# Optimization experiments

Measured on AMD Instinct MI355X. Metric: run time of the kernel, lower is better.

## Reference

```python
import jax, jax.numpy as jnp
import numpy as np

B, S, D, K = 16, 4096, 256, 1024


def setup_inputs() -> dict:
    key = jax.random.key(0)
    k1, k2 = jax.random.split(key)
    z_e = jax.random.normal(k1, (B, S, D), dtype=jnp.float32)
    # nn.Embedding weight initialized uniform(-1/K, 1/K)
    codebook = jax.random.uniform(k2, (K, D), dtype=jnp.float32,
                                  minval=-1.0 / K, maxval=1.0 / K)
    return {"z_e": z_e, "codebook": codebook}


def reference(z_e, codebook):
    # straight_through path of VQEmbedding
    d = codebook.shape[1]
    x = z_e.reshape(-1, d)                                   # [N, D]
    dist = (jnp.sum(x * x, axis=1, keepdims=True)
            + jnp.sum(codebook * codebook, axis=1)
            - 2.0 * (x @ codebook.T))                        # [N, K]
    idx = jnp.argmin(dist, axis=1)                           # [N]
    codes = jnp.take(codebook, idx, axis=0).reshape(z_e.shape)  # gather
    z_q = z_e + jax.lax.stop_gradient(codes - z_e)           # straight-through codes (detached codebook)
    z_q_bar = codes                                          # codes with grad to codebook
    return (z_q, z_q_bar)
```

## Files before the change

kernel.cpp:

```cpp
#include <hip/hip_runtime.h>
#include <stdint.h>

#define D 256
#define KCODES 1024
#define NROWS 65536

using int4v  = __attribute__((ext_vector_type(4))) int;
using f32x4v = __attribute__((ext_vector_type(4))) float;

__device__ __forceinline__ float rne_f(float x) { return __builtin_rintf(x); }

__device__ __forceinline__ void gl_lds16(const void* g, void* l) {
  __builtin_amdgcn_global_load_lds(
      (const __attribute__((address_space(1))) void*)g,
      (__attribute__((address_space(3))) void*)l, 16, 0, 0);
}

__device__ __forceinline__ void dig4(float t, int* d) {
  float f0 = rne_f(t);  float t1 = __fmul_rn(__fsub_rn(t, f0), 256.0f);
  float f1 = rne_f(t1); float t2 = __fmul_rn(__fsub_rn(t1, f1), 256.0f);
  float f2 = rne_f(t2); float t3 = __fmul_rn(__fsub_rn(t2, f2), 256.0f);
  float f3 = rne_f(t3);
  int d0 = (int)f0, d1 = (int)f1, d2 = (int)f2, d3 = (int)f3;
  if (d3 == 128) { d3 = -128; ++d2; }
  if (d2 == 128) { d2 = -128; ++d1; }
  if (d1 == 128) { d1 = -128; ++d0; }
  d[0] = d0; d[1] = d1; d[2] = d2; d[3] = d3;
}

__device__ __forceinline__ float np_block128_sumsq(const float* __restrict__ q) {
  float r[8], v[8];
  *(float4*)(v) = *(const float4*)(q);
  *(float4*)(v + 4) = *(const float4*)(q + 4);
#pragma unroll
  for (int j = 0; j < 8; ++j) r[j] = __fmul_rn(v[j], v[j]);
  for (int i = 8; i < 128; i += 8) {
    *(float4*)(v) = *(const float4*)(q + i);
    *(float4*)(v + 4) = *(const float4*)(q + i + 4);
#pragma unroll
    for (int j = 0; j < 8; ++j) r[j] = __fadd_rn(r[j], __fmul_rn(v[j], v[j]));
  }
  float t01 = __fadd_rn(r[0], r[1]);
  float t23 = __fadd_rn(r[2], r[3]);
  float t45 = __fadd_rn(r[4], r[5]);
  float t67 = __fadd_rn(r[6], r[7]);
  return __fadd_rn(__fadd_rn(t01, t23), __fadd_rn(t45, t67));
}
__device__ __forceinline__ float np_sumsq256(const float* __restrict__ q) {
  return __fadd_rn(np_block128_sumsq(q), np_block128_sumsq(q + 128));
}

__global__ __launch_bounds__(256) void prep_all(const float* __restrict__ z,
                                                const float* __restrict__ cb,
                                                float* __restrict__ c2,
                                                float* __restrict__ srow,
                                                char* __restrict__ cbd) {
  __shared__ float zs[64][260];
  const int bid = blockIdx.x;
  const int tid = threadIdx.x;
  if (bid < 1040) {
    const float* src; float* dst; int r0;
    if (bid < 1024) { r0 = bid * 64; src = z; dst = srow; }
    else            { r0 = (bid - 1024) * 64; src = cb; dst = c2; }
#pragma unroll
    for (int it = 0; it < 16; ++it) {
      int g = tid + it * 256, row = g >> 6, f4 = g & 63;
      *(float4*)(&zs[row][f4 * 4]) = *(const float4*)(src + (size_t)(r0 + row) * D + f4 * 4);
    }
    __syncthreads();
    if (tid < 64) dst[r0 + tid] = np_sumsq256(&zs[tid][0]);
    return;
  }
  int id = (bid - 1040) * 256 + tid;
  int n = id >> 4, kc = id & 15;
  int f = kc >> 2, kg = kc & 3, nt = n >> 5, c = n & 31;
  const float* src = cb + (size_t)n * D + kc * 16;
  float v[16];
  *(float4*)(v) = *(const float4*)(src);
  *(float4*)(v + 4) = *(const float4*)(src + 4);
  *(float4*)(v + 8) = *(const float4*)(src + 8);
  *(float4*)(v + 12) = *(const float4*)(src + 12);
  int dg[16][4];
#pragma unroll
  for (int e = 0; e < 16; ++e) dig4(v[e] * 65536.0f, dg[e]);
  size_t base = (size_t)nt * 8192 + f * 2048 + (c >> 4) * 1024 + kg * 256 + (c & 15) * 16;
#pragma unroll
  for (int p = 0; p < 4; ++p) {
    int4v wv;
#pragma unroll
    for (int wi = 0; wi < 4; ++wi)
      wv[wi] = (dg[wi * 4][p] & 255) | ((dg[wi * 4 + 1][p] & 255) << 8) |
               ((dg[wi * 4 + 2][p] & 255) << 16) | (dg[wi * 4 + 3][p] << 24);
    *(int4v*)(cbd + (size_t)p * (KCODES * 256) + base) = wv;
  }
}

#define BM 64
#define BN 16
#define NT (KCODES / BN)

#define MFI16(a, b, c) __builtin_amdgcn_mfma_i32_16x16x64_i8((a), (b), (c), 0, 0, 0)

__global__ __launch_bounds__(256, 4) void vq_mfma(
    const float* __restrict__ z, const float* __restrict__ cb,
    const float* __restrict__ c2g, const float* __restrict__ srowg,
    const char* __restrict__ cbd, float* __restrict__ out) {
  __shared__ alignas(16) char bbuf[2][16384];
  __shared__ float c2s[KCODES];
  __shared__ int bidx_s[BM];

  const int tid = threadIdx.x;
  const int lane = tid & 63;
  const int w = tid >> 6;
  const int r0 = blockIdx.x * BM;
  const int l15 = lane & 15, l4 = lane >> 4;

  c2s[tid] = c2g[tid];
  c2s[tid + 256] = c2g[tid + 256];
  c2s[tid + 512] = c2g[tid + 512];
  c2s[tid + 768] = c2g[tid + 768];

  float sr[4];
#pragma unroll
  for (int r = 0; r < 4; ++r) sr[r] = srowg[r0 + w * 16 + l4 * 4 + r];

  int4v Adig[4][4];
  {
    const float* zr = z + (size_t)(r0 + w * 16 + l15) * D + l4 * 16;
#pragma unroll
    for (int f = 0; f < 4; ++f) {
      float v[16];
      *(float4*)(v) = *(const float4*)(zr + f * 64);
      *(float4*)(v + 4) = *(const float4*)(zr + f * 64 + 4);
      *(float4*)(v + 8) = *(const float4*)(zr + f * 64 + 8);
      *(float4*)(v + 12) = *(const float4*)(zr + f * 64 + 12);
      int dg[16][4];
#pragma unroll
      for (int e = 0; e < 16; ++e) dig4(v[e] * 16.0f, dg[e]);
#pragma unroll
      for (int p = 0; p < 4; ++p) {
        int4v wv;
#pragma unroll
        for (int wi = 0; wi < 4; ++wi)
          wv[wi] = (dg[wi * 4][p] & 255) | ((dg[wi * 4 + 1][p] & 255) << 8) |
                   ((dg[wi * 4 + 2][p] & 255) << 16) | (dg[wi * 4 + 3][p] << 24);
        Adig[p][f] = wv;
      }
    }
  }

  const char* cbd_b = cbd;
#define STAGE(ntv, dstbase) do { \
    const char* s_ = cbd_b + (size_t)((ntv) >> 1) * 8192 + (tid >> 6) * 2048 + \
                     ((ntv) & 1) * 1024 + (tid & 63) * 16; \
    char* d_ = (dstbase) + (tid >> 6) * 1024 + (tid & 63) * 16; \
    gl_lds16(s_,          d_); \
    gl_lds16(s_ + 262144, d_ + 4096); \
    gl_lds16(s_ + 524288, d_ + 8192); \
    gl_lds16(s_ + 786432, d_ + 12288); \
  } while (0)

  float bd[4]; int bi[4];
#pragma unroll
  for (int r = 0; r < 4; ++r) { bd[r] = 3.4e38f; bi[r] = 0x7fffffff; }

  int4v acc[4];

  STAGE(0, &bbuf[0][0]);
  __syncthreads();

  for (int nt = 0; nt < NT; ++nt) {
    const char* cur = &bbuf[nt & 1][0];
    if (nt + 1 < NT) STAGE(nt + 1, &bbuf[(nt + 1) & 1][0]);
#pragma unroll
    for (int s = 0; s < 4; ++s) { int4v zz = {0, 0, 0, 0}; acc[s] = zz; }
#pragma unroll
    for (int kf = 0; kf < 4; ++kf) {
      const char* pb = cur + kf * 1024 + lane * 16;
      int4v B0 = *(const int4v*)(pb);
      int4v B1 = *(const int4v*)(pb + 4096);
      int4v B2 = *(const int4v*)(pb + 8192);
      int4v B3 = *(const int4v*)(pb + 12288);
      acc[1] = MFI16(Adig[0][kf], B1, acc[1]);
      acc[3] = MFI16(Adig[0][kf], B3, acc[3]);
      acc[2] = MFI16(Adig[0][kf], B2, acc[2]);
      acc[1] = MFI16(Adig[1][kf], B0, acc[1]);
      acc[3] = MFI16(Adig[1][kf], B2, acc[3]);
      acc[2] = MFI16(Adig[1][kf], B1, acc[2]);
      acc[0] = MFI16(Adig[0][kf], B0, acc[0]);
      acc[3] = MFI16(Adig[2][kf], B1, acc[3]);
      acc[2] = MFI16(Adig[2][kf], B0, acc[2]);
      acc[3] = MFI16(Adig[3][kf], B0, acc[3]);
    }
    {
      const int kc = nt * BN + l15;
      const float c2v = c2s[kc];
#pragma unroll
      for (int r = 0; r < 4; ++r) {
        int hi32 = acc[0][r] * 256 + acc[1][r];
        double lo_d = fma((double)acc[2][r], 256.0, (double)acc[3][r]);
        double md = fma((double)hi32, 65536.0, lo_d) * 0x1p-44;
        float mf = (float)md;
        float dist = __fsub_rn(__fadd_rn(sr[r], c2v), __fmul_rn(2.0f, mf));
        if (dist < bd[r]) { bd[r] = dist; bi[r] = kc; }
      }
    }
    __syncthreads();
  }

#pragma unroll
  for (int r = 0; r < 4; ++r) {
#pragma unroll
    for (int m = 1; m < 16; m <<= 1) {
      float od = __shfl_xor(bd[r], m);
      int oi = __shfl_xor(bi[r], m);
      if (od < bd[r] || (od == bd[r] && oi < bi[r])) { bd[r] = od; bi[r] = oi; }
    }
    if (l15 == 0) bidx_s[w * 16 + l4 * 4 + r] = bi[r];
  }
  __syncthreads();

  {
    float* out0 = out;
    float* out1 = out + (size_t)NROWS * D;
#pragma unroll
    for (int rr = 0; rr < 16; ++rr) {
      const int row_l = w * 16 + rr;
      const int grow = r0 + row_l;
      const int kb = bidx_s[row_l];
      f32x4v c4 = *(const f32x4v*)(cb + (size_t)kb * D + lane * 4);
      f32x4v z4 = *(const f32x4v*)(z + (size_t)grow * D + lane * 4);
      f32x4v q;
      q.x = __fadd_rn(z4.x, __fsub_rn(c4.x, z4.x));
      q.y = __fadd_rn(z4.y, __fsub_rn(c4.y, z4.y));
      q.z = __fadd_rn(z4.z, __fsub_rn(c4.z, z4.z));
      q.w = __fadd_rn(z4.w, __fsub_rn(c4.w, z4.w));
      __builtin_nontemporal_store(q, (f32x4v*)(out0 + (size_t)grow * D + lane * 4));
      __builtin_nontemporal_store(c4, (f32x4v*)(out1 + (size_t)grow * D + lane * 4));
    }
  }
}

__global__ void c2_kernel_fb(const float* __restrict__ cb, float* __restrict__ c2) {
  int k = blockIdx.x * blockDim.x + threadIdx.x;
  if (k < KCODES) c2[k] = np_sumsq256(cb + (size_t)k * D);
}

__global__ __launch_bounds__(256) void vq_fallback(const float* __restrict__ z,
                                                   const float* __restrict__ cb,
                                                   const float* __restrict__ c2,
                                                   float* __restrict__ out) {
  __shared__ float zs[64][260];
  __shared__ float cs[64][260];
  __shared__ float srow[64];
  __shared__ int bidx[64];
  const int tid = threadIdx.x;
  const int tx = tid & 15, ty = tid >> 4;
  const int r0 = blockIdx.x * 64;
#pragma unroll
  for (int it = 0; it < 16; ++it) {
    int g = tid + it * 256, row = g >> 6, f4 = g & 63;
    *(float4*)(&zs[row][f4 * 4]) = *(const float4*)(z + (size_t)(r0 + row) * D + f4 * 4);
  }
  __syncthreads();
  if (tid < 64) srow[tid] = np_sumsq256(&zs[tid][0]);
  float bd[4]; int bi[4];
#pragma unroll
  for (int j = 0; j < 4; ++j) { bd[j] = 3.4e38f; bi[j] = 0x7fffffff; }
  for (int t = 0; t < KCODES / 64; ++t) {
    __syncthreads();
#pragma unroll
    for (int it = 0; it < 16; ++it) {
      int g = tid + it * 256, row = g >> 6, f4 = g & 63;
      *(float4*)(&cs[row][f4 * 4]) = *(const float4*)(cb + (size_t)(t * 64 + row) * D + f4 * 4);
    }
    __syncthreads();
    double acc[4][4];
#pragma unroll
    for (int j = 0; j < 4; ++j)
#pragma unroll
      for (int i = 0; i < 4; ++i) acc[j][i] = 0.0;
#pragma unroll 2
    for (int d = 0; d < D; d += 4) {
      float4 a[4], b[4];
#pragma unroll
      for (int j = 0; j < 4; ++j) a[j] = *(const float4*)(&zs[ty + 16 * j][d]);
#pragma unroll
      for (int i = 0; i < 4; ++i) b[i] = *(const float4*)(&cs[tx + 16 * i][d]);
#pragma unroll
      for (int j = 0; j < 4; ++j)
#pragma unroll
        for (int i = 0; i < 4; ++i) {
          acc[j][i] += (double)a[j].x * (double)b[i].x;
          acc[j][i] += (double)a[j].y * (double)b[i].y;
          acc[j][i] += (double)a[j].z * (double)b[i].z;
          acc[j][i] += (double)a[j].w * (double)b[i].w;
        }
    }
#pragma unroll
    for (int j = 0; j < 4; ++j) {
      const float s = srow[ty + 16 * j];
#pragma unroll
      for (int i = 0; i < 4; ++i) {
        const int k = t * 64 + tx + 16 * i;
        const float m = (float)acc[j][i];
        const float dist = __fsub_rn(__fadd_rn(s, c2[k]), __fmul_rn(2.0f, m));
        if (dist < bd[j]) { bd[j] = dist; bi[j] = k; }
      }
    }
  }
  __syncthreads();
  float* red_d = &cs[0][0];
  int* red_i = (int*)&cs[20][0];
#pragma unroll
  for (int j = 0; j < 4; ++j) {
    red_d[(ty + 16 * j) * 16 + tx] = bd[j];
    red_i[(ty + 16 * j) * 16 + tx] = bi[j];
  }
  __syncthreads();
  if (tid < 64) {
    float best = red_d[tid * 16 + 0];
    int bsti = red_i[tid * 16 + 0];
    for (int x = 1; x < 16; ++x) {
      float d2 = red_d[tid * 16 + x]; int i2 = red_i[tid * 16 + x];
      if (d2 < best || (d2 == best && i2 < bsti)) { best = d2; bsti = i2; }
    }
    bidx[tid] = bsti;
  }
  __syncthreads();
  const int wid = tid >> 6, lane = tid & 63;
  float* out0 = out;
  float* out1 = out + (size_t)NROWS * D;
  for (int r = wid; r < 64; r += 4) {
    const int gr = r0 + r;
    const int kb = bidx[r];
    float4 c4 = *(const float4*)(cb + (size_t)kb * D + lane * 4);
    float4 z4 = *(const float4*)(&zs[r][lane * 4]);
    float4 q;
    q.x = __fadd_rn(z4.x, __fsub_rn(c4.x, z4.x));
    q.y = __fadd_rn(z4.y, __fsub_rn(c4.y, z4.y));
    q.z = __fadd_rn(z4.z, __fsub_rn(c4.z, z4.z));
    q.w = __fadd_rn(z4.w, __fsub_rn(c4.w, z4.w));
    *(float4*)(out0 + (size_t)gr * D + lane * 4) = q;
    *(float4*)(out1 + (size_t)gr * D + lane * 4) = c4;
  }
}

extern "C" void kernel_launch(void* const* d_in, const int* in_sizes, int n_in,
                              void* d_out, int out_size, void* d_ws, size_t ws_size,
                              hipStream_t stream) {
  const float* z = (const float*)d_in[0];
  const float* cb = (const float*)d_in[1];
  float* out = (float*)d_out;

  const size_t c2_off = 0;
  const size_t srow_off = 4096;
  const size_t cbd_off = 4096 + 262144;
  const size_t need = cbd_off + (size_t)4 * KCODES * 256;

  if (ws_size < need) {
    float* c2 = (float*)d_ws;
    c2_kernel_fb<<<KCODES / 256, 256, 0, stream>>>(cb, c2);
    vq_fallback<<<NROWS / 64, 256, 0, stream>>>(z, cb, c2, out);
    return;
  }

  float* c2 = (float*)((char*)d_ws + c2_off);
  float* srow = (float*)((char*)d_ws + srow_off);
  char* cbd = (char*)d_ws + cbd_off;

  prep_all<<<1104, 256, 0, stream>>>(z, cb, c2, srow, cbd);
  vq_mfma<<<NROWS / BM, 256, 0, stream>>>(z, cb, c2, srow, cbd, out);
}
```

Baseline: 175.9 us.

## Load codebook digits directly from global memory instead of LDS double buffer

Removes the LDS double-buffered staging of the int8 codebook digit tiles (global_load_lds plus per-iteration barriers). Each wave now reads its B fragments straight from global memory, relying on L2/L1 caching because every block reads the same codebook. This drops the per-tile __syncthreads and frees 32KB of LDS. The trade-off is exposed global-load latency with no explicit prefetch, so the MFMA chain may stall on loads. Launch bounds are relaxed from 4 to 3 waves per SIMD.

```diff
diff --git a/kernel.cpp b/kernel.cpp
--- a/kernel.cpp
+++ b/kernel.cpp
@@ -9,12 +9,6 @@
 using f32x4v = __attribute__((ext_vector_type(4))) float;
 
 __device__ __forceinline__ float rne_f(float x) { return __builtin_rintf(x); }
-
-__device__ __forceinline__ void gl_lds16(const void* g, void* l) {
-  __builtin_amdgcn_global_load_lds(
-      (const __attribute__((address_space(1))) void*)g,
-      (__attribute__((address_space(3))) void*)l, 16, 0, 0);
-}
 
 __device__ __forceinline__ void dig4(float t, int* d) {
   float f0 = rne_f(t);  float t1 = __fmul_rn(__fsub_rn(t, f0), 256.0f);
@@ -101,11 +95,10 @@
 
 #define MFI16(a, b, c) __builtin_amdgcn_mfma_i32_16x16x64_i8((a), (b), (c), 0, 0, 0)
 
-__global__ __launch_bounds__(256, 4) void vq_mfma(
+__global__ __launch_bounds__(256, 3) void vq_mfma(
     const float* __restrict__ z, const float* __restrict__ cb,
     const float* __restrict__ c2g, const float* __restrict__ srowg,
     const char* __restrict__ cbd, float* __restrict__ out) {
-  __shared__ alignas(16) char bbuf[2][16384];
   __shared__ float c2s[KCODES];
   __shared__ int bidx_s[BM];
 
@@ -149,38 +142,26 @@
     }
   }
 
-  const char* cbd_b = cbd;
-#define STAGE(ntv, dstbase) do { \
-    const char* s_ = cbd_b + (size_t)((ntv) >> 1) * 8192 + (tid >> 6) * 2048 + \
-                     ((ntv) & 1) * 1024 + (tid & 63) * 16; \
-    char* d_ = (dstbase) + (tid >> 6) * 1024 + (tid & 63) * 16; \
-    gl_lds16(s_,          d_); \
-    gl_lds16(s_ + 262144, d_ + 4096); \
-    gl_lds16(s_ + 524288, d_ + 8192); \
-    gl_lds16(s_ + 786432, d_ + 12288); \
-  } while (0)
+  __syncthreads();
 
   float bd[4]; int bi[4];
 #pragma unroll
   for (int r = 0; r < 4; ++r) { bd[r] = 3.4e38f; bi[r] = 0x7fffffff; }
 
   int4v acc[4];
-
-  STAGE(0, &bbuf[0][0]);
-  __syncthreads();
+  const char* cbd_b = cbd + lane * 16;
 
   for (int nt = 0; nt < NT; ++nt) {
-    const char* cur = &bbuf[nt & 1][0];
-    if (nt + 1 < NT) STAGE(nt + 1, &bbuf[(nt + 1) & 1][0]);
+    const char* tb = cbd_b + (size_t)(nt >> 1) * 8192 + (nt & 1) * 1024;
 #pragma unroll
     for (int s = 0; s < 4; ++s) { int4v zz = {0, 0, 0, 0}; acc[s] = zz; }
 #pragma unroll
     for (int kf = 0; kf < 4; ++kf) {
-      const char* pb = cur + kf * 1024 + lane * 16;
-      int4v B0 = *(const int4v*)(pb);
-      int4v B1 = *(const int4v*)(pb + 4096);
-      int4v B2 = *(const int4v*)(pb + 8192);
-      int4v B3 = *(const int4v*)(pb + 12288);
+      const char* pk = tb + kf * 2048;
+      int4v B0 = *(const int4v*)(pk);
+      int4v B1 = *(const int4v*)(pk + 262144);
+      int4v B2 = *(const int4v*)(pk + 524288);
+      int4v B3 = *(const int4v*)(pk + 786432);
       acc[1] = MFI16(Adig[0][kf], B1, acc[1]);
       acc[3] = MFI16(Adig[0][kf], B3, acc[3]);
       acc[2] = MFI16(Adig[0][kf], B2, acc[2]);
@@ -205,7 +186,6 @@
         if (dist < bd[r]) { bd[r] = dist; bi[r] = kc; }
       }
     }
-    __syncthreads();
   }
 
 #pragma unroll
```

After: 348.6 us. +98.2%, slower.

## Triple-buffer codebook tiles in LDS with counted vmcnt waits and MFMA priority

Applied to the files above, without the earlier changes.

Replaces the double-buffered LDS staging of codebook digit tiles with a three-buffer ring that prefetches two tiles ahead. It waits with explicit s_waitcnt vmcnt(4) plus a raw s_barrier instead of a full __syncthreads, so the load for the next-but-one tile stays in flight across the barrier. The MFMA block is wrapped in s_setprio to favour matrix issue. This adds 16KB of LDS per block, which may lower occupancy under launch_bounds(256,4), and the hand-written wait counts have to match the number of outstanding loads exactly.

```diff
diff --git a/kernel.cpp b/kernel.cpp
--- a/kernel.cpp
+++ b/kernel.cpp
@@ -105,7 +105,7 @@
     const float* __restrict__ z, const float* __restrict__ cb,
     const float* __restrict__ c2g, const float* __restrict__ srowg,
     const char* __restrict__ cbd, float* __restrict__ out) {
-  __shared__ alignas(16) char bbuf[2][16384];
+  __shared__ alignas(16) char bbuf[3][16384];
   __shared__ float c2s[KCODES];
   __shared__ int bidx_s[BM];
 
@@ -165,22 +165,28 @@
   for (int r = 0; r < 4; ++r) { bd[r] = 3.4e38f; bi[r] = 0x7fffffff; }
 
   int4v acc[4];
-
-  STAGE(0, &bbuf[0][0]);
-  __syncthreads();
+  char* pa = &bbuf[0][0];
+  char* pb = &bbuf[1][0];
+  char* pc = &bbuf[2][0];
+
+  STAGE(0, pa);
+  STAGE(1, pb);
+  asm volatile("s_waitcnt vmcnt(4) lgkmcnt(0)" ::: "memory");
+  __builtin_amdgcn_s_barrier();
+  __builtin_amdgcn_sched_barrier(0);
 
   for (int nt = 0; nt < NT; ++nt) {
-    const char* cur = &bbuf[nt & 1][0];
-    if (nt + 1 < NT) STAGE(nt + 1, &bbuf[(nt + 1) & 1][0]);
+    if (nt + 2 < NT) STAGE(nt + 2, pc);
 #pragma unroll
     for (int s = 0; s < 4; ++s) { int4v zz = {0, 0, 0, 0}; acc[s] = zz; }
 #pragma unroll
     for (int kf = 0; kf < 4; ++kf) {
-      const char* pb = cur + kf * 1024 + lane * 16;
-      int4v B0 = *(const int4v*)(pb);
-      int4v B1 = *(const int4v*)(pb + 4096);
-      int4v B2 = *(const int4v*)(pb + 8192);
-      int4v B3 = *(const int4v*)(pb + 12288);
+      const char* pk = pa + kf * 1024 + lane * 16;
+      int4v B0 = *(const int4v*)(pk);
+      int4v B1 = *(const int4v*)(pk + 4096);
+      int4v B2 = *(const int4v*)(pk + 8192);
+      int4v B3 = *(const int4v*)(pk + 12288);
+      __builtin_amdgcn_s_setprio(1);
       acc[1] = MFI16(Adig[0][kf], B1, acc[1]);
       acc[3] = MFI16(Adig[0][kf], B3, acc[3]);
       acc[2] = MFI16(Adig[0][kf], B2, acc[2]);
@@ -191,6 +197,7 @@
       acc[3] = MFI16(Adig[2][kf], B1, acc[3]);
       acc[2] = MFI16(Adig[2][kf], B0, acc[2]);
       acc[3] = MFI16(Adig[3][kf], B0, acc[3]);
+      __builtin_amdgcn_s_setprio(0);
     }
     {
       const int kc = nt * BN + l15;
@@ -205,7 +212,13 @@
         if (dist < bd[r]) { bd[r] = dist; bi[r] = kc; }
       }
     }
-    __syncthreads();
+    if (nt + 1 < NT) {
+      if (nt + 2 < NT) asm volatile("s_waitcnt vmcnt(4)" ::: "memory");
+      else             asm volatile("s_waitcnt vmcnt(0)" ::: "memory");
+      __builtin_amdgcn_s_barrier();
+      __builtin_amdgcn_sched_barrier(0);
+    }
+    char* tmp = pa; pa = pb; pb = pc; pc = tmp;
   }
 
 #pragma unroll
```

Measured after the change: 212.3 us. 20.7% more time.
